# Kernel optimization log

Hardware: AMD Instinct MI355X
Metric: run time of the kernel (lower is better)

## Reference

```python
import jax, jax.numpy as jnp
import numpy as np


def setup_inputs() -> dict:
    key = jax.random.key(0)
    x = jax.random.normal(key, (4, 4, 32, 256, 256), dtype=jnp.float32)
    return {"x": x}


def reference(x):
    # NonMaximaSuppression3d with kernel_size=(3,3,3) fast path:
    # a voxel survives iff it is strictly greater than all 26 neighbors;
    # border voxels (no full neighborhood) are always suppressed.
    B, CH, D, H, W = x.shape
    ct = x[..., 1:-1, 1:-1, 1:-1]  # interior centers [B,CH,D-2,H-2,W-2]
    mask_inner = jnp.ones(ct.shape, dtype=bool)
    for dz in range(3):
        for dy in range(3):
            for dx in range(3):
                if (dz, dy, dx) == (1, 1, 1):
                    continue
                neigh = x[..., dz:D - 2 + dz, dy:H - 2 + dy, dx:W - 2 + dx]
                mask_inner = mask_inner & (ct > neigh)
    mask = jnp.zeros(x.shape, dtype=bool).at[..., 1:-1, 1:-1, 1:-1].set(mask_inner)
    return x * mask.astype(x.dtype)
```

## Files before the change

### kernel.cpp

```cpp
#include <hip/hip_runtime.h>


typedef float v4f __attribute__((ext_vector_type(4)));

constexpr int W  = 256;
constexpr int H  = 256;
constexpr int D  = 32;
constexpr int SH = W;
constexpr int SD = W * H;
constexpr int HC = 8;
constexpr int HCHUNKS = H / HC;
constexpr int BC = 16;

__device__ __forceinline__ v4f vmax4(v4f a, v4f b) {
    return (v4f){fmaxf(a.x, b.x), fmaxf(a.y, b.y), fmaxf(a.z, b.z), fmaxf(a.w, b.w)};
}

__global__ __launch_bounds__(256) void nms3d_kernel(const float* __restrict__ x,
                                                    float* __restrict__ out) {
    const int wid  = (blockIdx.x << 2) | (threadIdx.x >> 6);
    const int lane = threadIdx.x & 63;
    const int hc   = wid & (HCHUNKS - 1);
    const int d    = (wid >> 5) & (D - 1);
    const int bc   = wid >> 10;
    const int col  = bc * (D * SD) + d * SD + (lane << 2);
    const int h0   = hc * HC;

    const v4f zero = (v4f){0.f, 0.f, 0.f, 0.f};

    if (d == 0 || d == D - 1) {
        #pragma unroll
        for (int i = 0; i < HC; ++i)
            __builtin_nontemporal_store(zero, (v4f*)(out + col + (h0 + i) * SH));
        return;
    }

    const float* xm = x + col - SD;
    const float* x0 = x + col;
    const float* xp = x + col + SD;

    v4f raw[10][3];
    v4f pm3[10];
    v4f pm2[10];
    v4f cen[10];

    #define LOADT(s) { int hh = h0 - 1 + (s); hh = hh < 0 ? 0 : (hh > H-1 ? H-1 : hh); \
        raw[s][0] = *(const v4f*)(xm + hh * SH); \
        raw[s][1] = *(const v4f*)(x0 + hh * SH); \
        raw[s][2] = *(const v4f*)(xp + hh * SH); }
    #define REDUCET(s) { pm2[s] = vmax4(raw[s][0], raw[s][2]); \
        pm3[s] = vmax4(pm2[s], raw[s][1]); cen[s] = raw[s][1]; }

    LOADT(0) LOADT(1) LOADT(2) LOADT(3) LOADT(4)
    REDUCET(0) REDUCET(1) REDUCET(2)

    #pragma unroll
    for (int i = 0; i < HC; ++i) {
        if (i + 5 <= 9) LOADT(i + 5)
        REDUCET(i + 3)

        const int h = h0 + i;
        v4f v8 = vmax4(vmax4(pm3[i], pm2[i + 1]), pm3[i + 2]);
        float l8 = __shfl_up(v8.w, 1);
        float r8 = __shfl_down(v8.x, 1);
        const v4f c = cen[i + 1];
        float lc = __shfl_up(c.w, 1);
        float rc = __shfl_down(c.x, 1);

        float n0 = fmaxf(fmaxf(l8,   v8.x), v8.y);
        float n1 = fmaxf(fmaxf(v8.x, v8.y), v8.z);
        float n2 = fmaxf(fmaxf(v8.y, v8.z), v8.w);
        float n3 = fmaxf(fmaxf(v8.z, v8.w), r8);
        n0 = fmaxf(n0, fmaxf(lc,  c.y));
        n1 = fmaxf(n1, fmaxf(c.x, c.z));
        n2 = fmaxf(n2, fmaxf(c.y, c.w));
        n3 = fmaxf(n3, fmaxf(c.z, rc));

        const bool hv = (h > 0) && (h < H - 1);
        v4f o;
        o.x = (hv && lane > 0  && c.x > n0) ? c.x : 0.f;
        o.y = (hv && c.y > n1) ? c.y : 0.f;
        o.z = (hv && c.z > n2) ? c.z : 0.f;
        o.w = (hv && lane < 63 && c.w > n3) ? c.w : 0.f;
        __builtin_nontemporal_store(o, (v4f*)(out + col + h * SH));
    }
    #undef LOADT
    #undef REDUCET
}

extern "C" void kernel_launch(void* const* d_in, const int* in_sizes, int n_in,
                              void* d_out, int out_size, void* d_ws, size_t ws_size,
                              hipStream_t stream) {
    const float* x = (const float*)d_in[0];
    float* out = (float*)d_out;
    const int grid = (BC * D * HCHUNKS) / 4;
    nms3d_kernel<<<grid, 256, 0, stream>>>(x, out);
}
```

Baseline: 235.9 us.

## Process four depth slices per warp to reuse loaded neighbor slices

Each wavefront now computes KD=4 consecutive depth slices for its 8-row H chunk, loading KD+2 depth planes with a rolling 3-row register window instead of re-reading three planes per output slice. This cuts redundant global/L2 reads of neighboring depth slices and folds the border-slice zeroing into a validity mask. It reduces the grid by 4x and raises register pressure, with less load prefetch depth per step, which may lower latency hiding.

After: 237.0 us. No clear change (+0.5%).

```diff
diff --git a/kernel.cpp b/kernel.cpp
--- a/kernel.cpp
+++ b/kernel.cpp
@@ -8,9 +8,11 @@
 constexpr int D  = 32;
 constexpr int SH = W;
 constexpr int SD = W * H;
+constexpr int KD = 4;
 constexpr int HC = 8;
-constexpr int HCHUNKS = H / HC;
 constexpr int BC = 16;
+constexpr int DG = D / KD;
+constexpr int HG = H / HC;
 
 __device__ __forceinline__ v4f vmax4(v4f a, v4f b) {
     return (v4f){fmaxf(a.x, b.x), fmaxf(a.y, b.y), fmaxf(a.z, b.z), fmaxf(a.w, b.w)};
@@ -20,72 +22,85 @@
                                                     float* __restrict__ out) {
     const int wid  = (blockIdx.x << 2) | (threadIdx.x >> 6);
     const int lane = threadIdx.x & 63;
-    const int hc   = wid & (HCHUNKS - 1);
-    const int d    = (wid >> 5) & (D - 1);
-    const int bc   = wid >> 10;
-    const int col  = bc * (D * SD) + d * SD + (lane << 2);
+    const int hc   = wid & (HG - 1);
+    const int dg   = (wid >> 5) & (DG - 1);
+    const int bc   = wid >> 8;
+    const int d0   = dg * KD;
     const int h0   = hc * HC;
 
-    const v4f zero = (v4f){0.f, 0.f, 0.f, 0.f};
+    const float* vol  = x   + bc * (D * SD) + (lane << 2);
+    float*       ovol = out + bc * (D * SD) + (lane << 2);
 
-    if (d == 0 || d == D - 1) {
-        #pragma unroll
-        for (int i = 0; i < HC; ++i)
-            __builtin_nontemporal_store(zero, (v4f*)(out + col + (h0 + i) * SH));
-        return;
+    const float* base[KD + 2];
+    #pragma unroll
+    for (int j = 0; j < KD + 2; ++j) {
+        int p = d0 - 1 + j;
+        p = p < 0 ? 0 : (p > D - 1 ? D - 1 : p);
+        base[j] = vol + p * SD;
     }
 
-    const float* xm = x + col - SD;
-    const float* x0 = x + col;
-    const float* xp = x + col + SD;
+    bool dvalid[KD];
+    #pragma unroll
+    for (int k = 0; k < KD; ++k) {
+        const int dd = d0 + k;
+        dvalid[k] = (dd > 0) && (dd < D - 1);
+    }
 
-    v4f raw[10][3];
-    v4f pm3[10];
-    v4f pm2[10];
-    v4f cen[10];
-
-    #define LOADT(s) { int hh = h0 - 1 + (s); hh = hh < 0 ? 0 : (hh > H-1 ? H-1 : hh); \
-        raw[s][0] = *(const v4f*)(xm + hh * SH); \
-        raw[s][1] = *(const v4f*)(x0 + hh * SH); \
-        raw[s][2] = *(const v4f*)(xp + hh * SH); }
-    #define REDUCET(s) { pm2[s] = vmax4(raw[s][0], raw[s][2]); \
-        pm3[s] = vmax4(pm2[s], raw[s][1]); cen[s] = raw[s][1]; }
-
-    LOADT(0) LOADT(1) LOADT(2) LOADT(3) LOADT(4)
-    REDUCET(0) REDUCET(1) REDUCET(2)
+    v4f r[KD + 2][3];
+    {
+        const int hm = (h0 - 1 < 0) ? 0 : h0 - 1;
+        #pragma unroll
+        for (int j = 0; j < KD + 2; ++j) r[j][0] = *(const v4f*)(base[j] + hm * SH);
+        #pragma unroll
+        for (int j = 0; j < KD + 2; ++j) r[j][1] = *(const v4f*)(base[j] + h0 * SH);
+    }
 
     #pragma unroll
     for (int i = 0; i < HC; ++i) {
-        if (i + 5 <= 9) LOADT(i + 5)
-        REDUCET(i + 3)
+        const int h  = h0 + i;
+        const int s0 = i % 3, s1 = (i + 1) % 3, s2 = (i + 2) % 3;
 
-        const int h = h0 + i;
-        v4f v8 = vmax4(vmax4(pm3[i], pm2[i + 1]), pm3[i + 2]);
-        float l8 = __shfl_up(v8.w, 1);
-        float r8 = __shfl_down(v8.x, 1);
-        const v4f c = cen[i + 1];
-        float lc = __shfl_up(c.w, 1);
-        float rc = __shfl_down(c.x, 1);
+        const int hp = (h + 1 > H - 1) ? H - 1 : h + 1;
+        #pragma unroll
+        for (int j = 0; j < KD + 2; ++j)
+            r[j][s2] = *(const v4f*)(base[j] + hp * SH);
 
-        float n0 = fmaxf(fmaxf(l8,   v8.x), v8.y);
-        float n1 = fmaxf(fmaxf(v8.x, v8.y), v8.z);
-        float n2 = fmaxf(fmaxf(v8.y, v8.z), v8.w);
-        float n3 = fmaxf(fmaxf(v8.z, v8.w), r8);
-        n0 = fmaxf(n0, fmaxf(lc,  c.y));
-        n1 = fmaxf(n1, fmaxf(c.x, c.z));
-        n2 = fmaxf(n2, fmaxf(c.y, c.w));
-        n3 = fmaxf(n3, fmaxf(c.z, rc));
+        v4f a2[KD + 2], a3[KD + 2];
+        #pragma unroll
+        for (int j = 0; j < KD + 2; ++j) {
+            a2[j] = vmax4(r[j][s0], r[j][s2]);
+            a3[j] = vmax4(a2[j], r[j][s1]);
+        }
 
-        const bool hv = (h > 0) && (h < H - 1);
-        v4f o;
-        o.x = (hv && lane > 0  && c.x > n0) ? c.x : 0.f;
-        o.y = (hv && c.y > n1) ? c.y : 0.f;
-        o.z = (hv && c.z > n2) ? c.z : 0.f;
-        o.w = (hv && lane < 63 && c.w > n3) ? c.w : 0.f;
-        __builtin_nontemporal_store(o, (v4f*)(out + col + h * SH));
+        const bool hvalid = (h > 0) && (h < H - 1);
+
+        #pragma unroll
+        for (int k = 0; k < KD; ++k) {
+            v4f v8 = vmax4(vmax4(a3[k], a3[k + 2]), a2[k + 1]);
+            const v4f c = r[k + 1][s1];
+            float l8 = __shfl_up(v8.w, 1);
+            float r8 = __shfl_down(v8.x, 1);
+            float lc = __shfl_up(c.w, 1);
+            float rc = __shfl_down(c.x, 1);
+
+            float n0 = fmaxf(fmaxf(l8,   v8.x), v8.y);
+            float n1 = fmaxf(fmaxf(v8.x, v8.y), v8.z);
+            float n2 = fmaxf(fmaxf(v8.y, v8.z), v8.w);
+            float n3 = fmaxf(fmaxf(v8.z, v8.w), r8);
+            n0 = fmaxf(n0, fmaxf(lc,  c.y));
+            n1 = fmaxf(n1, fmaxf(c.x, c.z));
+            n2 = fmaxf(n2, fmaxf(c.y, c.w));
+            n3 = fmaxf(n3, fmaxf(c.z, rc));
+
+            const bool v = hvalid && dvalid[k];
+            v4f o;
+            o.x = (v && lane > 0  && c.x > n0) ? c.x : 0.f;
+            o.y = (v && c.y > n1) ? c.y : 0.f;
+            o.z = (v && c.z > n2) ? c.z : 0.f;
+            o.w = (v && lane < 63 && c.w > n3) ? c.w : 0.f;
+            __builtin_nontemporal_store(o, (v4f*)(ovol + (d0 + k) * SD + h * SH));
+        }
     }
-    #undef LOADT
-    #undef REDUCET
 }
 
 extern "C" void kernel_launch(void* const* d_in, const int* in_sizes, int n_in,
@@ -93,6 +108,6 @@
                               hipStream_t stream) {
     const float* x = (const float*)d_in[0];
     float* out = (float*)d_out;
-    const int grid = (BC * D * HCHUNKS) / 4;
+    const int grid = (BC * DG * HG) / 4;
     nms3d_kernel<<<grid, 256, 0, stream>>>(x, out);
 }
```
